# Performance work log

Hardware: AMD Instinct MI355X
Metric: run time of the kernel (lower is better)

## Reference

```python
import jax, jax.numpy as jnp
import numpy as np

HEAD_NUM = 16

def setup_inputs() -> dict:
    key = jax.random.key(0)
    ks = jax.random.split(key, 5)
    B, N, D = 2, 2048, 1024
    x = jax.random.normal(ks[0], (B, N, D), dtype=jnp.float32)
    scale = 0.02
    W_q = jax.random.normal(ks[1], (D, D), dtype=jnp.float32) * scale
    W_k = jax.random.normal(ks[2], (D, D), dtype=jnp.float32) * scale
    W_v = jax.random.normal(ks[3], (D, D), dtype=jnp.float32) * scale
    W_o = jax.random.normal(ks[4], (D, D), dtype=jnp.float32) * scale
    return {"x": x, "W_q": W_q, "W_k": W_k, "W_v": W_v, "W_o": W_o}

def reference(x, W_q, W_k, W_v, W_o):
    B, N, D = x.shape
    H = HEAD_NUM
    hd = D // H  # head_dim
    inv_sqrt_hd = 1.0 / np.sqrt(hd).astype(np.float32)

    def split_head(t):
        # einops 'b n (d h) -> b h n d' : head index is the INNER factor
        return t.reshape(B, N, hd, H).transpose(0, 3, 1, 2)  # [B,H,N,hd]

    # nn.Linear(bias=False): y = x @ W.T
    Q = split_head(x @ W_q.T)
    K = split_head(x @ W_k.T)
    V = split_head(x @ W_v.T)

    scores = jnp.einsum('bhnd,bhmd->bhnm', Q, K) * inv_sqrt_hd  # [B,H,N,N]
    attn = jax.nn.softmax(scores, axis=-1)
    heads = jnp.einsum('bhnm,bhmd->bhnd', attn, V)  # [B,H,N,hd]

    # einops 'b h n d -> b n (h d)' : head index is the OUTER factor here
    concat = heads.transpose(0, 2, 1, 3).reshape(B, N, D)
    return concat @ W_o.T
```

## Files before the change

### kernel.cpp

```cpp
#include <hip/hip_runtime.h>
#include <hip/hip_bf16.h>

typedef __bf16 bf16_t;
typedef __attribute__((ext_vector_type(8))) __bf16 bf16x8;
typedef __attribute__((ext_vector_type(4))) __bf16 bf16x4;
typedef __attribute__((ext_vector_type(4))) float f32x4;
typedef __attribute__((ext_vector_type(16))) float f32x16;

#define MFMA16(A,B,C) __builtin_amdgcn_mfma_f32_16x16x32_bf16((A),(B),(C),0,0,0)
#define MFMA32(A,B,C) __builtin_amdgcn_mfma_f32_32x32x16_bf16((A),(B),(C),0,0,0)

#define BATCH 2
#define SEQ 2048
#define DMODEL 1024
#define NHEAD 16
#define HDIM 64
#define MROWS (BATCH * SEQ)

__device__ __forceinline__ void async16(const bf16_t* g, bf16_t* l) {
    __builtin_amdgcn_global_load_lds(
        (const __attribute__((address_space(1))) unsigned int*)g,
        (__attribute__((address_space(3))) unsigned int*)l, 16, 0, 0);
}

__device__ __forceinline__ bf16x8 ldsA32(const bf16_t* base, int row, int chunk) {
    return *(const bf16x8*)&base[row * 32 + ((chunk ^ ((row >> 1) & 3)) << 3)];
}

__device__ __forceinline__ unsigned pk(float a, float b) {
    union { unsigned u; bf16_t h[2]; } t;
    t.h[0] = (bf16_t)a;
    t.h[1] = (bf16_t)b;
    return t.u;
}

__device__ __forceinline__ void plane32_swap(unsigned& d, unsigned& s) {
    asm("v_permlane32_swap_b32 %0, %1" : "+v"(d), "+v"(s));
}

__device__ __forceinline__ void sm_pack(const f32x16& st, float* rsp, bf16x8* pf) {
    float pexp[16];
#pragma unroll
    for (int r = 0; r < 16; ++r)
        pexp[r] = __builtin_amdgcn_exp2f(st[r]);
    rsp[0] += pexp[0] + pexp[4] + pexp[8] + pexp[12];
    rsp[1] += pexp[1] + pexp[5] + pexp[9] + pexp[13];
    rsp[2] += pexp[2] + pexp[6] + pexp[10] + pexp[14];
    rsp[3] += pexp[3] + pexp[7] + pexp[11] + pexp[15];
#pragma unroll
    for (int s1 = 0; s1 < 2; ++s1) {
        unsigned lo01 = pk(pexp[8 * s1 + 0], pexp[8 * s1 + 1]);
        unsigned lo23 = pk(pexp[8 * s1 + 2], pexp[8 * s1 + 3]);
        unsigned hi01 = pk(pexp[8 * s1 + 4], pexp[8 * s1 + 5]);
        unsigned hi23 = pk(pexp[8 * s1 + 6], pexp[8 * s1 + 7]);
        plane32_swap(lo01, hi01);
        plane32_swap(lo23, hi23);
        union { bf16x8 v; unsigned u[4]; } outv;
        outv.u[0] = lo01;
        outv.u[1] = lo23;
        outv.u[2] = hi01;
        outv.u[3] = hi23;
        pf[s1] = outv.v;
    }
}

__global__ void split_kernel(const float* __restrict__ x, const float* __restrict__ Wq,
                             const float* __restrict__ Wk, const float* __restrict__ Wv,
                             const float* __restrict__ Wo, bf16_t* __restrict__ xh,
                             bf16_t* __restrict__ wh) {
    int blk = blockIdx.x;
    if (blk < 4096) {
        int i = blk * 256 + threadIdx.x;
        f32x4 v = ((const f32x4*)x)[i];
        bf16x4 h;
#pragma unroll
        for (int c = 0; c < 4; ++c) h[c] = (bf16_t)v[c];
        ((bf16x4*)xh)[i] = h;
        return;
    }
    int e = blk - 4096;
    int z = e >> 10;
    int i = (e & 1023) * 256 + threadIdx.x;
    const float* src = (z == 0) ? Wq : (z == 1) ? Wk : (z == 2) ? Wv : Wo;
    const float scale = (z == 0) ? 0.125f * 1.44269504088896f : 1.0f;
    int row = i >> 8, col4 = i & 255;
    int r_src;
    if (z < 3) {
        int h = row >> 6, d = row & 63;
        r_src = 16 * d + h;
    } else {
        r_src = row;
    }
    f32x4 v = ((const f32x4*)src)[r_src * 256 + col4];
    bf16x4 h4;
#pragma unroll
    for (int c = 0; c < 4; ++c) h4[c] = (bf16_t)(v[c] * scale);
    ((bf16x4*)(wh + (size_t)z * DMODEL * DMODEL))[i] = h4;
}

__global__ __launch_bounds__(256)
void gemm_qkv_kernel(const bf16_t* __restrict__ Ah, const bf16_t* __restrict__ Bh0,
                     bf16_t* __restrict__ Coh0, bf16_t* __restrict__ Vt,
                     int M, int Nn, int Kk) {
    __shared__ __align__(16) bf16_t smem[2][8192];

    const int id = blockIdx.x;
    const int xcd = id & 7;
    const int t = id >> 3;
    const int n0i = t & 7;
    const int u = t >> 3;
    const int z = u >> 2;
    const int m0g = u & 3;
    const int m0 = (m0g * 8 + xcd) * 128;
    const int n0 = n0i * 128;

    const bf16_t* Bh = Bh0 + (size_t)z * Nn * Kk;
    const int tid = threadIdx.x;
    const int wave = tid >> 6, lane = tid & 63, lq = lane >> 4, ln = lane & 15;
    const int wr = wave >> 1, wc = wave & 1;

    const bf16_t* g_ptr[4];
    int l_off[4];
#pragma unroll
    for (int q = 0; q < 4; ++q) {
        int e = wave * 4 + q;
        int a = e >> 3, uu = e & 7;
        int C = uu * 64 + lane;
        int r = C >> 2, p = C & 3;
        int c = p ^ ((r >> 1) & 3);
        g_ptr[q] = (a == 0 ? Ah + (size_t)(m0 + r) * Kk
                           : Bh + (size_t)(n0 + r) * Kk) + c * 8;
        l_off[q] = a * 4096 + uu * 512;
    }

    f32x4 acc[4][4] = {};

#pragma unroll
    for (int q = 0; q < 4; ++q)
        async16(g_ptr[q], &smem[0][l_off[q]]);

    const int NIT = Kk / 32;
    for (int j = 0; j < NIT; ++j) {
        __syncthreads();
        if (j + 1 < NIT) {
#pragma unroll
            for (int q = 0; q < 4; ++q)
                async16(g_ptr[q] + (j + 1) * 32, &smem[(j + 1) & 1][l_off[q]]);
        }
        const bf16_t* cur = smem[j & 1];

        bf16x8 ah[4], bh[4];
#pragma unroll
        for (int tt = 0; tt < 4; ++tt) {
            ah[tt] = ldsA32(cur, wr * 64 + tt * 16 + ln, lq);
            bh[tt] = ldsA32(cur + 4096, wc * 64 + tt * 16 + ln, lq);
        }
#pragma unroll
        for (int tm = 0; tm < 4; ++tm)
#pragma unroll
            for (int tn = 0; tn < 4; ++tn)
                acc[tm][tn] = MFMA16(ah[tm], bh[tn], acc[tm][tn]);
    }

    if (z != 2) {
#pragma unroll
        for (int tm = 0; tm < 4; ++tm)
#pragma unroll
            for (int tn = 0; tn < 4; ++tn)
#pragma unroll
                for (int p = 0; p < 4; ++p) {
                    int gm = m0 + wr * 64 + tm * 16 + lq * 4 + p;
                    int gn = n0 + wc * 64 + tn * 16 + ln;
                    Coh0[(size_t)z * M * Nn + (size_t)gm * Nn + gn] =
                        (bf16_t)acc[tm][tn][p];
                }
    } else {
#pragma unroll
        for (int tm = 0; tm < 4; ++tm)
#pragma unroll
            for (int tn = 0; tn < 4; ++tn) {
                int gn = n0 + wc * 64 + tn * 16 + ln;
                int hh = gn >> 6, dd = gn & 63;
                int gm0 = m0 + wr * 64 + tm * 16 + lq * 4;
                int bb = gm0 >> 11, nn = gm0 & 2047;
                bf16x4 v4;
#pragma unroll
                for (int p = 0; p < 4; ++p) v4[p] = (bf16_t)acc[tm][tn][p];
                *(bf16x4*)&Vt[(((size_t)(bb * NHEAD + hh)) * HDIM + dd) * SEQ + nn] = v4;
            }
    }
}

__global__ __launch_bounds__(256)
void gemm_out_kernel(const bf16_t* __restrict__ Ah, const bf16_t* __restrict__ Bh,
                     float* __restrict__ Cf, int M, int Nn, int Kk) {
    __shared__ __align__(16) bf16_t smem[2][6144];

    const int id = blockIdx.x;
    const int xcd = id & 7;
    const int t = id >> 3;
    const int n0i = t & 7;
    const int m0g = t >> 3;
    const int m0 = (m0g * 8 + xcd) * 64;
    const int n0 = n0i * 128;

    const int tid = threadIdx.x;
    const int wave = tid >> 6, lane = tid & 63, lq = lane >> 4, ln = lane & 15;
    const int wr = wave >> 1, wc = wave & 1;

    const bf16_t* g_ptr[3];
    int l_off[3];
#pragma unroll
    for (int q = 0; q < 3; ++q) {
        int e = wave * 3 + q;
        const bf16_t* arr;
        int u, rowbase, lb;
        if (e < 4) { arr = Ah; u = e;     rowbase = m0; lb = 0; }
        else       { arr = Bh; u = e - 4; rowbase = n0; lb = 2048; }
        int r = u * 16 + (lane >> 2), p = lane & 3;
        int c = p ^ ((r >> 1) & 3);
        g_ptr[q] = arr + (size_t)(rowbase + r) * Kk + c * 8;
        l_off[q] = lb + u * 512;
    }

    f32x4 acc[2][4] = {};

#pragma unroll
    for (int q = 0; q < 3; ++q)
        async16(g_ptr[q], &smem[0][l_off[q]]);

    const int NIT = Kk / 32;
    for (int j = 0; j < NIT; ++j) {
        __syncthreads();
        if (j + 1 < NIT) {
#pragma unroll
            for (int q = 0; q < 3; ++q)
                async16(g_ptr[q] + (j + 1) * 32, &smem[(j + 1) & 1][l_off[q]]);
        }
        const bf16_t* cur = smem[j & 1];

        bf16x8 ah[2], bh[4];
#pragma unroll
        for (int tt = 0; tt < 2; ++tt)
            ah[tt] = ldsA32(cur, wr * 32 + tt * 16 + ln, lq);
#pragma unroll
        for (int tt = 0; tt < 4; ++tt)
            bh[tt] = ldsA32(cur + 2048, wc * 64 + tt * 16 + ln, lq);
#pragma unroll
        for (int tm = 0; tm < 2; ++tm)
#pragma unroll
            for (int tn = 0; tn < 4; ++tn)
                acc[tm][tn] = MFMA16(ah[tm], bh[tn], acc[tm][tn]);
    }

#pragma unroll
    for (int tm = 0; tm < 2; ++tm)
#pragma unroll
        for (int tn = 0; tn < 4; ++tn)
#pragma unroll
            for (int p = 0; p < 4; ++p) {
                int gm = m0 + wr * 32 + tm * 16 + lq * 4 + p;
                int gn = n0 + wc * 64 + tn * 16 + ln;
                Cf[(size_t)gm * Nn + gn] = acc[tm][tn][p];
            }
}

__global__ __launch_bounds__(512, 1)
void attn_kernel(const bf16_t* __restrict__ Qh, const bf16_t* __restrict__ Kh,
                 const bf16_t* __restrict__ Vt, bf16_t* __restrict__ Ch) {
    __shared__ __align__(16) bf16_t smem[2][2][8192];

    const int id = blockIdx.x;
    const int bh = ((id >> 6) << 3) | (id & 7);
    const int qt = (id >> 3) & 7;
    const int b = bh >> 4, h = bh & 15;
    const int q0 = qt * 256;
    const int tid = threadIdx.x;
    const int g = tid >> 8;
    const int wv = (tid >> 6) & 3;
    const int lane = tid & 63;
    const int ln32 = lane & 31, hl = lane >> 5;

    bf16x8 qfh[2][4];
#pragma unroll
    for (int qs = 0; qs < 2; ++qs) {
        size_t qrow = ((size_t)(b * SEQ + q0 + wv * 64 + qs * 32 + ln32)) * DMODEL +
                      h * HDIM + hl * 8;
#pragma unroll
        for (int c = 0; c < 4; ++c)
            qfh[qs][c] = *(const bf16x8*)&Qh[qrow + c * 16];
    }

    const int xrow = ln32 * 64;
    int xc[4];
#pragma unroll
    for (int c = 0; c < 4; ++c)
        xc[c] = (((2 * c + hl) ^ (ln32 & 7)) << 3) + xrow;

    bf16_t* gsm = &smem[g][0][0];
    const bf16_t* g_cur[4];
    int l_off[4];
    size_t g_step[4];
#pragma unroll
    for (int q = 0; q < 4; ++q) {
        int e = wv * 4 + q;
        int a = e >> 3, u = e & 7;
        int r = u * 8 + (lane >> 3), p = lane & 7;
        int c = p ^ (r & 7);
        if (a == 0) {
            g_cur[q] = Kh + ((size_t)(b * SEQ + g * 1024 + r)) * DMODEL +
                       h * HDIM + c * 8;
            l_off[q] = u * 512;
            g_step[q] = (size_t)64 * DMODEL;
        } else {
            g_cur[q] = Vt + ((size_t)(bh * HDIM + r)) * SEQ + g * 1024 + c * 8;
            l_off[q] = 4096 + u * 512;
            g_step[q] = 64;
        }
    }

    f32x16 o[2][2];
#pragma unroll
    for (int qs = 0; qs < 2; ++qs)
#pragma unroll
        for (int dt = 0; dt < 2; ++dt)
#pragma unroll
            for (int r = 0; r < 16; ++r) o[qs][dt][r] = 0.0f;
    f32x16 zacc;
#pragma unroll
    for (int r = 0; r < 16; ++r) zacc[r] = 0.0f;
    float rsA[4] = {0.f, 0.f, 0.f, 0.f};
    float rsB[4] = {0.f, 0.f, 0.f, 0.f};

#pragma unroll
    for (int q = 0; q < 4; ++q) {
        async16(g_cur[q], gsm + l_off[q]);
        g_cur[q] += g_step[q];
    }

    for (int j = 0; j < 16; ++j) {
        __syncthreads();
        if (j < 15) {
#pragma unroll
            for (int q = 0; q < 4; ++q) {
                async16(g_cur[q], gsm + ((j + 1) & 1) * 8192 + l_off[q]);
                g_cur[q] += g_step[q];
            }
        }
        const bf16_t* Kc = gsm + (j & 1) * 8192;
        const bf16_t* Vc = Kc + 4096;

        bf16x8 pfA[4], pfB[4];
#pragma unroll
        for (int kt = 0; kt < 2; ++kt) {
            bf16x8 kh[4];
#pragma unroll
            for (int c = 0; c < 4; ++c)
                kh[c] = *(const bf16x8*)&Kc[kt * 2048 + xc[c]];
            __builtin_amdgcn_s_setprio(1);
            f32x16 s0 = MFMA32(kh[0], qfh[0][0], zacc);
            f32x16 s1 = MFMA32(kh[0], qfh[1][0], zacc);
#pragma unroll
            for (int c = 1; c < 4; ++c)
                s0 = MFMA32(kh[c], qfh[0][c], s0);
#pragma unroll
            for (int c = 1; c < 4; ++c)
                s1 = MFMA32(kh[c], qfh[1][c], s1);
            __builtin_amdgcn_s_setprio(0);
            sm_pack(s0, rsA, &pfA[kt * 2]);
            sm_pack(s1, rsB, &pfB[kt * 2]);
        }
        __builtin_amdgcn_s_setprio(1);
#pragma unroll
        for (int s = 0; s < 4; ++s) {
            bf16x8 va0 = *(const bf16x8*)&Vc[xc[s]];
            bf16x8 va1 = *(const bf16x8*)&Vc[2048 + xc[s]];
            o[0][0] = MFMA32(va0, pfA[s], o[0][0]);
            o[0][1] = MFMA32(va1, pfA[s], o[0][1]);
            o[1][0] = MFMA32(va0, pfB[s], o[1][0]);
            o[1][1] = MFMA32(va1, pfB[s], o[1][1]);
        }
        __builtin_amdgcn_s_setprio(0);
    }

    float rs[2];
    rs[0] = (rsA[0] + rsA[1]) + (rsA[2] + rsA[3]);
    rs[1] = (rsB[0] + rsB[1]) + (rsB[2] + rsB[3]);
#pragma unroll
    for (int qs = 0; qs < 2; ++qs)
        rs[qs] += __shfl_xor(rs[qs], 32);

    __syncthreads();
    float* cbuf = (float*)smem;
    float* rbuf = cbuf + 8192;
#pragma unroll
    for (int dt = 0; dt < 2; ++dt) {
        if (g == 1) {
#pragma unroll
            for (int qs = 0; qs < 2; ++qs)
#pragma unroll
                for (int r = 0; r < 16; ++r) {
                    int d = (r & 3) + 8 * (r >> 2) + 4 * hl;
                    cbuf[d * 256 + wv * 64 + qs * 32 + ln32] = o[qs][dt][r];
                }
            if (dt == 0 && hl == 0) {
                rbuf[wv * 64 + ln32] = rs[0];
                rbuf[wv * 64 + 32 + ln32] = rs[1];
            }
        }
        __syncthreads();
        if (g == 0) {
#pragma unroll
            for (int qs = 0; qs < 2; ++qs) {
#pragma unroll
                for (int r = 0; r < 16; ++r) {
                    int d = (r & 3) + 8 * (r >> 2) + 4 * hl;
                    o[qs][dt][r] += cbuf[d * 256 + wv * 64 + qs * 32 + ln32];
                }
                if (dt == 0) rs[qs] += rbuf[wv * 64 + qs * 32 + ln32];
            }
        }
        __syncthreads();
    }
    float inv[2];
    inv[0] = (g == 0) ? 1.0f / rs[0] : 0.0f;
    inv[1] = (g == 0) ? 1.0f / rs[1] : 0.0f;

    float* fbuf = (float*)smem;
#pragma unroll
    for (int dh = 0; dh < 2; ++dh) {
        if (g == 0) {
#pragma unroll
            for (int qs = 0; qs < 2; ++qs)
#pragma unroll
                for (int r = 0; r < 16; ++r) {
                    int d_loc = (r & 3) + 8 * (r >> 2) + 4 * hl;
                    fbuf[(wv * 64 + qs * 32 + ln32) * 33 + d_loc] =
                        o[qs][dh][r] * inv[qs];
                }
        }
        __syncthreads();
        {
            int gw = tid >> 6;
#pragma unroll
            for (int qq = 0; qq < 16; ++qq) {
                int qrow = gw * 32 + hl * 16 + qq;
                float v = fbuf[qrow * 33 + ln32];
                size_t gidx = ((size_t)(b * SEQ + q0 + qrow)) * DMODEL +
                              h * HDIM + dh * 32 + ln32;
                Ch[gidx] = (bf16_t)v;
            }
        }
        __syncthreads();
    }
}

extern "C" void kernel_launch(void* const* d_in, const int* in_sizes, int n_in,
                              void* d_out, int out_size, void* d_ws, size_t ws_size,
                              hipStream_t stream) {
    const float* x  = (const float*)d_in[0];
    const float* Wq = (const float*)d_in[1];
    const float* Wk = (const float*)d_in[2];
    const float* Wv = (const float*)d_in[3];
    const float* Wo = (const float*)d_in[4];
    float* out = (float*)d_out;

    char* ws = (char*)d_ws;
    size_t off = 0;
    auto alloc = [&](size_t bytes) -> bf16_t* {
        bf16_t* p = (bf16_t*)(ws + off);
        off += (bytes + 255) & ~(size_t)255;
        return p;
    };
    const size_t XE = (size_t)MROWS * DMODEL;
    const size_t WE = (size_t)DMODEL * DMODEL;

    bf16_t* xh  = alloc(XE * 2);
    bf16_t* wh  = alloc(4 * WE * 2);
    bf16_t* qnh = alloc(3 * XE * 2);
    bf16_t* vth = alloc(XE * 2);
    bf16_t* ch  = alloc(XE * 2);
    (void)ws_size; (void)in_sizes; (void)n_in; (void)out_size;

    split_kernel<<<8192, 256, 0, stream>>>(x, Wq, Wk, Wv, Wo, xh, wh);

    gemm_qkv_kernel<<<768, 256, 0, stream>>>(xh, wh, qnh, vth, MROWS, DMODEL, DMODEL);

    attn_kernel<<<256, 512, 0, stream>>>(qnh, qnh + XE, vth, ch);

    gemm_out_kernel<<<512, 256, 0, stream>>>(ch, wh + 3 * WE, out, MROWS, DMODEL, DMODEL);
}
```

Baseline: 173.2 us.

## Enlarge QKV GEMM tiles to 256x256 with 512 threads and K=64 stages

Restructures the fused QKV projection GEMM to use 256x256 output tiles per workgroup, 8 waves, and 64-wide K steps with a new XOR-swizzled LDS layout. It also treats the three weight matrices as one concatenated N=3072 dimension, which reduces the grid to 192 blocks, and wraps the MFMA bursts in s_setprio. The aim is more operand reuse per LDS load and fewer global loads per FLOP. In exchange it uses 128KB of LDS and 128 accumulator registers per thread, allows only one block per CU, and launches fewer blocks than there are CUs, which may cost occupancy.

```diff
diff --git a/kernel.cpp b/kernel.cpp
--- a/kernel.cpp
+++ b/kernel.cpp
@@ -98,94 +98,109 @@
     ((bf16x4*)(wh + (size_t)z * DMODEL * DMODEL))[i] = h4;
 }
 
-__global__ __launch_bounds__(256)
+__global__ __launch_bounds__(512, 1)
 void gemm_qkv_kernel(const bf16_t* __restrict__ Ah, const bf16_t* __restrict__ Bh0,
-                     bf16_t* __restrict__ Coh0, bf16_t* __restrict__ Vt,
-                     int M, int Nn, int Kk) {
-    __shared__ __align__(16) bf16_t smem[2][8192];
+                     bf16_t* __restrict__ Coh0, bf16_t* __restrict__ Vt) {
+    __shared__ __align__(16) bf16_t smem[2][32768];
 
     const int id = blockIdx.x;
-    const int xcd = id & 7;
-    const int t = id >> 3;
-    const int n0i = t & 7;
-    const int u = t >> 3;
-    const int z = u >> 2;
-    const int m0g = u & 3;
-    const int m0 = (m0g * 8 + xcd) * 128;
-    const int n0 = n0i * 128;
-
-    const bf16_t* Bh = Bh0 + (size_t)z * Nn * Kk;
+    const int wgid = (id & 7) * 24 + (id >> 3);
+    const int m0 = (wgid / 12) * 256;
+    const int n0 = (wgid % 12) * 256;
+
     const int tid = threadIdx.x;
     const int wave = tid >> 6, lane = tid & 63, lq = lane >> 4, ln = lane & 15;
-    const int wr = wave >> 1, wc = wave & 1;
-
-    const bf16_t* g_ptr[4];
-    int l_off[4];
-#pragma unroll
-    for (int q = 0; q < 4; ++q) {
-        int e = wave * 4 + q;
-        int a = e >> 3, uu = e & 7;
-        int C = uu * 64 + lane;
-        int r = C >> 2, p = C & 3;
-        int c = p ^ ((r >> 1) & 3);
-        g_ptr[q] = (a == 0 ? Ah + (size_t)(m0 + r) * Kk
-                           : Bh + (size_t)(n0 + r) * Kk) + c * 8;
-        l_off[q] = a * 4096 + uu * 512;
-    }
-
-    f32x4 acc[4][4] = {};
-
-#pragma unroll
-    for (int q = 0; q < 4; ++q)
+    const int wr = wave >> 2, wc = wave & 3;
+
+    const bf16_t* g_ptr[8];
+    int l_off[8];
+#pragma unroll
+    for (int q = 0; q < 8; ++q) {
+        int a = q >> 2, u = q & 3;
+        int r = u * 64 + wave * 8 + (lane >> 3);
+        int c = (lane & 7) ^ (r & 7);
+        g_ptr[q] = (a == 0 ? Ah + (size_t)(m0 + r) * 1024
+                           : Bh0 + (size_t)(n0 + r) * 1024) + c * 8;
+        l_off[q] = a * 16384 + u * 4096 + wave * 512;
+    }
+
+    int xc2[2];
+#pragma unroll
+    for (int s = 0; s < 2; ++s)
+        xc2[s] = (((s * 4 + lq) ^ (ln & 7)) << 3) + ln * 64;
+
+    f32x4 acc[8][4] = {};
+
+#pragma unroll
+    for (int q = 0; q < 8; ++q)
         async16(g_ptr[q], &smem[0][l_off[q]]);
 
-    const int NIT = Kk / 32;
-    for (int j = 0; j < NIT; ++j) {
-        __syncthreads();
-        if (j + 1 < NIT) {
-#pragma unroll
-            for (int q = 0; q < 4; ++q)
-                async16(g_ptr[q] + (j + 1) * 32, &smem[(j + 1) & 1][l_off[q]]);
-        }
-        const bf16_t* cur = smem[j & 1];
-
-        bf16x8 ah[4], bh[4];
-#pragma unroll
-        for (int tt = 0; tt < 4; ++tt) {
-            ah[tt] = ldsA32(cur, wr * 64 + tt * 16 + ln, lq);
-            bh[tt] = ldsA32(cur + 4096, wc * 64 + tt * 16 + ln, lq);
-        }
-#pragma unroll
-        for (int tm = 0; tm < 4; ++tm)
-#pragma unroll
-            for (int tn = 0; tn < 4; ++tn)
-                acc[tm][tn] = MFMA16(ah[tm], bh[tn], acc[tm][tn]);
-    }
-
+    for (int j = 0; j < 16; ++j) {
+        __syncthreads();
+        if (j + 1 < 16) {
+#pragma unroll
+            for (int q = 0; q < 8; ++q)
+                async16(g_ptr[q] + (j + 1) * 64, &smem[(j + 1) & 1][l_off[q]]);
+        }
+        const bf16_t* cur = &smem[j & 1][0];
+
+        const bf16_t* curB = cur + 16384 + wc * 64 * 64;
+        bf16x8 bh[4][2];
+#pragma unroll
+        for (int nr = 0; nr < 4; ++nr)
+#pragma unroll
+            for (int s = 0; s < 2; ++s)
+                bh[nr][s] = *(const bf16x8*)&curB[nr * 16 * 64 + xc2[s]];
+
+        const bf16_t* curA = cur + wr * 128 * 64;
+#pragma unroll
+        for (int ph = 0; ph < 4; ++ph) {
+            bf16x8 ah[2][2];
+#pragma unroll
+            for (int mr = 0; mr < 2; ++mr)
+#pragma unroll
+                for (int s = 0; s < 2; ++s)
+                    ah[mr][s] = *(const bf16x8*)
+                        &curA[(ph * 32 + mr * 16) * 64 + xc2[s]];
+            __builtin_amdgcn_s_setprio(1);
+#pragma unroll
+            for (int s = 0; s < 2; ++s)
+#pragma unroll
+                for (int mr = 0; mr < 2; ++mr)
+#pragma unroll
+                    for (int nr = 0; nr < 4; ++nr)
+                        acc[ph * 2 + mr][nr] =
+                            MFMA16(ah[mr][s], bh[nr][s], acc[ph * 2 + mr][nr]);
+            __builtin_amdgcn_s_setprio(0);
+        }
+    }
+
+    const int z = n0 >> 10;
+    const int nn0 = n0 & 1023;
     if (z != 2) {
-#pragma unroll
-        for (int tm = 0; tm < 4; ++tm)
-#pragma unroll
-            for (int tn = 0; tn < 4; ++tn)
+        bf16_t* Co = Coh0 + (size_t)z * (size_t)MROWS * DMODEL;
+#pragma unroll
+        for (int am = 0; am < 8; ++am)
+#pragma unroll
+            for (int nr = 0; nr < 4; ++nr)
 #pragma unroll
                 for (int p = 0; p < 4; ++p) {
-                    int gm = m0 + wr * 64 + tm * 16 + lq * 4 + p;
-                    int gn = n0 + wc * 64 + tn * 16 + ln;
-                    Coh0[(size_t)z * M * Nn + (size_t)gm * Nn + gn] =
-                        (bf16_t)acc[tm][tn][p];
+                    int gm = m0 + wr * 128 + am * 16 + lq * 4 + p;
+                    int gn = nn0 + wc * 64 + nr * 16 + ln;
+                    Co[(size_t)gm * DMODEL + gn] = (bf16_t)acc[am][nr][p];
                 }
     } else {
 #pragma unroll
-        for (int tm = 0; tm < 4; ++tm)
-#pragma unroll
-            for (int tn = 0; tn < 4; ++tn) {
-                int gn = n0 + wc * 64 + tn * 16 + ln;
+        for (int am = 0; am < 8; ++am)
+#pragma unroll
+            for (int nr = 0; nr < 4; ++nr) {
+                int gn = nn0 + wc * 64 + nr * 16 + ln;
                 int hh = gn >> 6, dd = gn & 63;
-                int gm0 = m0 + wr * 64 + tm * 16 + lq * 4;
+                int gm0 = m0 + wr * 128 + am * 16 + lq * 4;
                 int bb = gm0 >> 11, nn = gm0 & 2047;
                 bf16x4 v4;
 #pragma unroll
-                for (int p = 0; p < 4; ++p) v4[p] = (bf16_t)acc[tm][tn][p];
+                for (int p = 0; p < 4; ++p) v4[p] = (bf16_t)acc[am][nr][p];
                 *(bf16x4*)&Vt[(((size_t)(bb * NHEAD + hh)) * HDIM + dd) * SEQ + nn] = v4;
             }
     }
@@ -484,7 +499,7 @@
 
     split_kernel<<<8192, 256, 0, stream>>>(x, Wq, Wk, Wv, Wo, xh, wh);
 
-    gemm_qkv_kernel<<<768, 256, 0, stream>>>(xh, wh, qnh, vth, MROWS, DMODEL, DMODEL);
+    gemm_qkv_kernel<<<192, 512, 0, stream>>>(xh, wh, qnh, vth);
 
     attn_kernel<<<256, 512, 0, stream>>>(qnh, qnh + XE, vth, ch);
 
```

After: 173.5 us. Within noise of the previous version (+0.2%).
